# Kernel tuning notes

Hardware: AMD Instinct MI355X
Metric: run time of the kernel (lower is better)

Reference implementation:

```python
import jax, jax.numpy as jnp
import numpy as np

B, S, D, H = 8, 2048, 1024, 4
HD = D // H


def _layernorm(x, w, b, eps=1e-5):
    mu = jnp.mean(x, axis=-1, keepdims=True)
    var = jnp.mean((x - mu) ** 2, axis=-1, keepdims=True)
    return (x - mu) * jax.lax.rsqrt(var + eps) * w + b


def setup_inputs() -> dict:
    key = jax.random.key(0)
    ks = jax.random.split(key, 10)
    s = 1.0 / np.sqrt(D)
    return {
        "text_representation": jax.random.normal(ks[0], (B, S, D), jnp.float32),
        "image_representation": jax.random.normal(ks[1], (B, S, D), jnp.float32),
        "ln_t_w": jnp.ones((D,), jnp.float32),
        "ln_t_b": jnp.zeros((D,), jnp.float32),
        "ln_i_w": jnp.ones((D,), jnp.float32),
        "ln_i_b": jnp.zeros((D,), jnp.float32),
        "Wa": jax.random.uniform(ks[2], (H, HD, D), jnp.float32, -s, s),
        "Wa_b": jax.random.uniform(ks[3], (H, HD), jnp.float32, -s, s),
        "Wq": jax.random.uniform(ks[4], (H, HD, D), jnp.float32, -s, s),
        "Wq_b": jax.random.uniform(ks[5], (H, HD), jnp.float32, -s, s),
        "sim_w": jax.random.uniform(ks[6], (HD, 1), jnp.float32, -1.0, 1.0),
        "sim_b": jax.random.uniform(ks[7], (HD,), jnp.float32, -1.0, 1.0),
        "fc_w": jax.random.uniform(ks[8], (1, H * HD), jnp.float32, -s, s),
        "fc_b": jax.random.uniform(ks[9], (1,), jnp.float32, -s, s),
    }


def reference(text_representation, image_representation, ln_t_w, ln_t_b,
              ln_i_w, ln_i_b, Wa, Wa_b, Wq, Wq_b, sim_w, sim_b, fc_w, fc_b):
    eps_cos = 1e-6
    text_rep = _layernorm(text_representation, ln_t_w, ln_t_b)   # [B,S,D]
    image_rep = _layernorm(image_representation, ln_i_w, ln_i_b)  # [B,S,D]
    # cosine similarity along last dim (torch-style norm clamping)
    tn = jnp.maximum(jnp.linalg.norm(text_rep, axis=-1), eps_cos)
    im = jnp.maximum(jnp.linalg.norm(image_rep, axis=-1), eps_cos)
    per_pos_sim = jnp.sum(text_rep * image_rep, axis=-1) / (tn * im)  # [B,S]
    global_sim = jnp.mean(per_pos_sim, axis=1, keepdims=True)          # [B,1]
    text_global = jnp.mean(text_rep, axis=1)    # [B,D]
    image_global = jnp.mean(image_rep, axis=1)  # [B,D]
    gate_a = jnp.einsum('bd,hkd->bhk', text_global, Wa) + Wa_b    # [B,H,HD]
    gate_q = jnp.einsum('bd,hkd->bhk', image_global, Wq) + Wq_b   # [B,H,HD]
    sim_feat = global_sim * sim_w[:, 0] + sim_b                   # [B,HD]
    gates = jax.nn.relu(gate_a + gate_q + sim_feat[:, None, :])   # [B,H,HD]
    combined = gates.reshape(gates.shape[0], H * HD)              # [B,H*HD]
    final_gate = jax.nn.sigmoid(combined @ fc_w.T + fc_b)         # [B,1]
    g = final_gate[:, :, None]                                    # [B,1,1]
    return g * text_rep + (1.0 - g) * image_rep
```

## Files before the change

kernel.cpp:

```cpp
#include <hip/hip_runtime.h>
#include <math.h>

#define BB 8
#define SS 2048
#define DD 1024
#define HH 4
#define HDD 256
#define NROW (BB*SS)

#define GG 32
#define NBLK (NROW/GG)

#define OFF_TG    0
#define OFF_IG    (BB*DD)
#define OFF_SIM   (2*BB*DD)
#define OFF_LOGIT (OFF_SIM + BB)
#define OFF_CNT   (OFF_LOGIT + BB)
#define WS_CLEAR  (OFF_CNT + 2)

#define GF 8
#define NSLF (NROW/GF)
#define F_MU_T 0
#define F_RS_T NROW
#define F_MU_I (2*NROW)
#define F_RS_I (3*NROW)
#define F_PT   (4*NROW)
#define F_PI   (F_PT + NSLF*DD)
#define F_PS   (F_PI + NSLF*DD)
#define F_TG   (F_PS + NSLF)
#define F_IG   (F_TG + BB*DD)
#define F_SIM  (F_IG + BB*DD)
#define F_LOGIT (F_SIM + BB)

__device__ __forceinline__ float wred(float v) {
#pragma unroll
  for (int m = 32; m > 0; m >>= 1) v += __shfl_xor(v, m, 64);
  return v;
}
__device__ __forceinline__ float hsum(const float4 v) { return v.x+v.y+v.z+v.w; }
__device__ __forceinline__ float hsq(const float4 v)  { return v.x*v.x+v.y*v.y+v.z*v.z+v.w*v.w; }
__device__ __forceinline__ float hdot(const float4 a, const float4 b) {
  return a.x*b.x + a.y*b.y + a.z*b.z + a.w*b.w;
}

__global__ __launch_bounds__(256, 2) void fused(
    const float* __restrict__ text, const float* __restrict__ image,
    const float* __restrict__ wt, const float* __restrict__ bt,
    const float* __restrict__ wi, const float* __restrict__ bi,
    const float* __restrict__ Wa, const float* __restrict__ Wab,
    const float* __restrict__ Wq, const float* __restrict__ Wqb,
    const float* __restrict__ simw, const float* __restrict__ simb,
    const float* __restrict__ fcw, const float* __restrict__ fcb,
    float* __restrict__ ws, float* __restrict__ out)
{
  const int blk  = blockIdx.x;
  const int tid  = threadIdx.x;
  const int lane = tid & 63;
  const int wv   = tid >> 6;
  const int row0 = blk * GG;
  const int b    = blk >> 6;

  __shared__ float smu_t[GG], srs_t[GG], smu_i[GG], srs_i[GG];
  __shared__ float sAcc[2][4][DD];
  __shared__ float ssim[4];
  __shared__ float red3[4][4][BB];

  int* c1 = (int*)(ws + OFF_CNT);
  int* c2 = c1 + 1;

  {
    const int cb = lane << 2;
    float4 Wt[4], Bt[4], Wi4[4], Bi4[4];
#pragma unroll
    for (int j = 0; j < 4; ++j) {
      Wt[j]  = *(const float4*)(wt + j*256 + cb);
      Bt[j]  = *(const float4*)(bt + j*256 + cb);
      Wi4[j] = *(const float4*)(wi + j*256 + cb);
      Bi4[j] = *(const float4*)(bi + j*256 + cb);
    }
    float4 tga[4], iga[4];
#pragma unroll
    for (int j = 0; j < 4; ++j) {
      tga[j] = make_float4(0.f,0.f,0.f,0.f);
      iga[j] = make_float4(0.f,0.f,0.f,0.f);
    }
    float sim_loc = 0.f;
    const float invD = 1.f/DD;
    const int rbase = row0 + wv*8;

    float4 tb[2][4], ib[2][4];
    {
      const float* tr = text  + (size_t)rbase*DD + cb;
      const float* ir = image + (size_t)rbase*DD + cb;
#pragma unroll
      for (int j = 0; j < 4; ++j) {
        tb[0][j] = *(const float4*)(tr + j*256);
        ib[0][j] = *(const float4*)(ir + j*256);
      }
    }

#pragma unroll 2
    for (int r = 0; r < 8; ++r) {
      const int cur = r & 1, nxt = cur ^ 1;
      if (r < 7) {
        const float* tr = text  + (size_t)(rbase + r + 1)*DD + cb;
        const float* ir = image + (size_t)(rbase + r + 1)*DD + cb;
#pragma unroll
        for (int j = 0; j < 4; ++j) {
          tb[nxt][j] = *(const float4*)(tr + j*256);
          ib[nxt][j] = *(const float4*)(ir + j*256);
        }
      }

      float st=0.f, qt=0.f, si=0.f, qi=0.f;
#pragma unroll
      for (int j = 0; j < 4; ++j) {
        st += hsum(tb[cur][j]);  qt += hsq(tb[cur][j]);
        si += hsum(ib[cur][j]);  qi += hsq(ib[cur][j]);
      }
      st = wred(st); qt = wred(qt); si = wred(si); qi = wred(qi);
      const float mt = st*invD, rt = rsqrtf(qt*invD - mt*mt + 1e-5f);
      const float mi = si*invD, ri = rsqrtf(qi*invD - mi*mi + 1e-5f);
      if (lane == 0) {
        smu_t[wv*8+r]=mt; srs_t[wv*8+r]=rt;
        smu_i[wv*8+r]=mi; srs_i[wv*8+r]=ri;
      }

      float dot=0.f, nt=0.f, ni=0.f;
#pragma unroll
      for (int j = 0; j < 4; ++j) {
        float4 tn, iv;
        tn.x = (tb[cur][j].x-mt)*rt*Wt[j].x + Bt[j].x;
        tn.y = (tb[cur][j].y-mt)*rt*Wt[j].y + Bt[j].y;
        tn.z = (tb[cur][j].z-mt)*rt*Wt[j].z + Bt[j].z;
        tn.w = (tb[cur][j].w-mt)*rt*Wt[j].w + Bt[j].w;
        iv.x = (ib[cur][j].x-mi)*ri*Wi4[j].x + Bi4[j].x;
        iv.y = (ib[cur][j].y-mi)*ri*Wi4[j].y + Bi4[j].y;
        iv.z = (ib[cur][j].z-mi)*ri*Wi4[j].z + Bi4[j].z;
        iv.w = (ib[cur][j].w-mi)*ri*Wi4[j].w + Bi4[j].w;
        tga[j].x += tn.x; tga[j].y += tn.y; tga[j].z += tn.z; tga[j].w += tn.w;
        iga[j].x += iv.x; iga[j].y += iv.y; iga[j].z += iv.z; iga[j].w += iv.w;
        dot += hdot(tn, iv); nt += hsq(tn); ni += hsq(iv);
      }
      dot = wred(dot); nt = wred(nt); ni = wred(ni);
      sim_loc += dot / (fmaxf(sqrtf(nt),1e-6f) * fmaxf(sqrtf(ni),1e-6f));
    }

#pragma unroll
    for (int j = 0; j < 4; ++j) {
      *(float4*)&sAcc[0][wv][j*256 + cb] = tga[j];
      *(float4*)&sAcc[1][wv][j*256 + cb] = iga[j];
    }
    if (lane == 0) ssim[wv] = sim_loc;
    __syncthreads();

    const int c0 = tid << 2;
    float4 vt = make_float4(0.f,0.f,0.f,0.f);
    float4 vi = make_float4(0.f,0.f,0.f,0.f);
#pragma unroll
    for (int w = 0; w < 4; ++w) {
      const float4 a = *(const float4*)&sAcc[0][w][c0];
      vt.x += a.x; vt.y += a.y; vt.z += a.z; vt.w += a.w;
      const float4 e = *(const float4*)&sAcc[1][w][c0];
      vi.x += e.x; vi.y += e.y; vi.z += e.z; vi.w += e.w;
    }
    atomicAdd(&ws[OFF_TG + b*DD + c0 + 0], vt.x);
    atomicAdd(&ws[OFF_TG + b*DD + c0 + 1], vt.y);
    atomicAdd(&ws[OFF_TG + b*DD + c0 + 2], vt.z);
    atomicAdd(&ws[OFF_TG + b*DD + c0 + 3], vt.w);
    atomicAdd(&ws[OFF_IG + b*DD + c0 + 0], vi.x);
    atomicAdd(&ws[OFF_IG + b*DD + c0 + 1], vi.y);
    atomicAdd(&ws[OFF_IG + b*DD + c0 + 2], vi.z);
    atomicAdd(&ws[OFF_IG + b*DD + c0 + 3], vi.w);
    if (tid == 0) {
      atomicAdd(&ws[OFF_SIM + b], ssim[0]+ssim[1]+ssim[2]+ssim[3]);
    }
  }

  __syncthreads();
  if (tid == 0) {
    __hip_atomic_fetch_add(c1, 1, __ATOMIC_RELEASE, __HIP_MEMORY_SCOPE_AGENT);
  }

  if (blk < 256) {
    if (tid == 0) {
      while (__hip_atomic_load(c1, __ATOMIC_RELAXED, __HIP_MEMORY_SCOPE_AGENT) < NBLK)
        __builtin_amdgcn_s_sleep(8);
      __threadfence();
    }
    __syncthreads();

    const int d0 = tid << 2;
    const int r0 = blk * 4;
    for (int rr = 0; rr < 4; ++rr) {
      const int r = r0 + rr;
      const float4 a4 = *(const float4*)(Wa + (size_t)r*DD + d0);
      const float4 q4 = *(const float4*)(Wq + (size_t)r*DD + d0);
      float acc[BB];
#pragma unroll
      for (int bq = 0; bq < BB; ++bq) {
        const float4 t = *(const float4*)(ws + OFF_TG + bq*DD + d0);
        const float4 i = *(const float4*)(ws + OFF_IG + bq*DD + d0);
        acc[bq] = hdot(a4, t) + hdot(q4, i);
      }
#pragma unroll
      for (int bq = 0; bq < BB; ++bq) {
        acc[bq] = wred(acc[bq]);
        if (lane == 0) red3[rr][wv][bq] = acc[bq];
      }
    }
    __syncthreads();
    if (tid < BB) {
      const int bq = tid;
      const float inv = 1.f/SS;
      const float gs = ws[OFF_SIM + bq] * inv;
      float part = 0.f;
#pragma unroll
      for (int rr = 0; rr < 4; ++rr) {
        const int r = r0 + rr;
        const int k = r & 255;
        const float v = (red3[rr][0][bq] + red3[rr][1][bq] + red3[rr][2][bq] + red3[rr][3][bq]) * inv;
        float gate = v + Wab[r] + Wqb[r] + gs*simw[k] + simb[k];
        gate = fmaxf(gate, 0.f);
        part += gate * fcw[r];
      }
      atomicAdd(&ws[OFF_LOGIT + bq], part);
    }
    __syncthreads();
    if (tid == 0) {
      __hip_atomic_fetch_add(c2, 1, __ATOMIC_RELEASE, __HIP_MEMORY_SCOPE_AGENT);
    }
  }

  if (tid == 0) {
    while (__hip_atomic_load(c2, __ATOMIC_RELAXED, __HIP_MEMORY_SCOPE_AGENT) < 256)
      __builtin_amdgcn_s_sleep(8);
    __threadfence();
  }
  __syncthreads();

  {
    const int d0 = tid << 2;
    const float4 wt4 = *(const float4*)(wt + d0);
    const float4 bt4 = *(const float4*)(bt + d0);
    const float4 wi4 = *(const float4*)(wi + d0);
    const float4 bi4 = *(const float4*)(bi + d0);
    const float g  = 1.f / (1.f + expf(-(ws[OFF_LOGIT + b] + fcb[0])));
    const float gi = 1.f - g;

    float4 tg[2][4], ig[2][4];
#pragma unroll
    for (int r = 0; r < 4; ++r) {
      tg[0][r] = *(const float4*)(text  + (size_t)(row0+r)*DD + d0);
      ig[0][r] = *(const float4*)(image + (size_t)(row0+r)*DD + d0);
    }
#pragma unroll 2
    for (int gidx = 0; gidx < 8; ++gidx) {
      const int cur = gidx & 1, nxt = cur ^ 1;
      if (gidx < 7) {
        const int nr = row0 + (gidx+1)*4;
#pragma unroll
        for (int r = 0; r < 4; ++r) {
          tg[nxt][r] = *(const float4*)(text  + (size_t)(nr+r)*DD + d0);
          ig[nxt][r] = *(const float4*)(image + (size_t)(nr+r)*DD + d0);
        }
      }
      const int rr = gidx*4;
#pragma unroll
      for (int r = 0; r < 4; ++r) {
        const float mt = smu_t[rr+r], rt = srs_t[rr+r];
        const float mi = smu_i[rr+r], ri = srs_i[rr+r];
        const float gt = g*rt, gii = gi*ri;
        float4 o;
        o.x = gt*(tg[cur][r].x-mt)*wt4.x + g*bt4.x + gii*(ig[cur][r].x-mi)*wi4.x + gi*bi4.x;
        o.y = gt*(tg[cur][r].y-mt)*wt4.y + g*bt4.y + gii*(ig[cur][r].y-mi)*wi4.y + gi*bi4.y;
        o.z = gt*(tg[cur][r].z-mt)*wt4.z + g*bt4.z + gii*(ig[cur][r].z-mi)*wi4.z + gi*bi4.z;
        o.w = gt*(tg[cur][r].w-mt)*wt4.w + g*bt4.w + gii*(ig[cur][r].w-mi)*wi4.w + gi*bi4.w;
        *(float4*)(out + (size_t)(row0+rr+r)*DD + d0) = o;
      }
    }
  }
}

__global__ __launch_bounds__(256) void k1_stats(
    const float* __restrict__ text, const float* __restrict__ image,
    const float* __restrict__ wt, const float* __restrict__ bt,
    const float* __restrict__ wi, const float* __restrict__ bi,
    float* __restrict__ ws)
{
  const int g    = blockIdx.x;
  const int tid  = threadIdx.x;
  const int lane = tid & 63;
  const int wv   = tid >> 6;
  const int d0   = tid << 2;
  const int row0 = g * GF;

  __shared__ float red1[4][8];
  __shared__ float red2[4][6];

  const float4 wt4 = *(const float4*)(wt + d0);
  const float4 bt4 = *(const float4*)(bt + d0);
  const float4 wi4 = *(const float4*)(wi + d0);
  const float4 bi4 = *(const float4*)(bi + d0);

  float4 tga = make_float4(0.f,0.f,0.f,0.f);
  float4 iga = make_float4(0.f,0.f,0.f,0.f);
  float sim_loc = 0.f;

  for (int r = 0; r < GF; r += 2) {
    const size_t base0 = (size_t)(row0 + r) * DD + d0;
    const size_t base1 = base0 + DD;
    const float4 t0 = *(const float4*)(text  + base0);
    const float4 i0 = *(const float4*)(image + base0);
    const float4 t1 = *(const float4*)(text  + base1);
    const float4 i1 = *(const float4*)(image + base1);

    float a0 = hsum(t0), a1 = hsq(t0), a2 = hsum(i0), a3 = hsq(i0);
    float a4 = hsum(t1), a5 = hsq(t1), a6 = hsum(i1), a7 = hsq(i1);
    a0 = wred(a0); a1 = wred(a1); a2 = wred(a2); a3 = wred(a3);
    a4 = wred(a4); a5 = wred(a5); a6 = wred(a6); a7 = wred(a7);
    if (lane == 0) {
      red1[wv][0]=a0; red1[wv][1]=a1; red1[wv][2]=a2; red1[wv][3]=a3;
      red1[wv][4]=a4; red1[wv][5]=a5; red1[wv][6]=a6; red1[wv][7]=a7;
    }
    __syncthreads();
    float s[8];
#pragma unroll
    for (int q = 0; q < 8; ++q) s[q] = red1[0][q]+red1[1][q]+red1[2][q]+red1[3][q];
    const float invD = 1.f/DD;
    const float mt0 = s[0]*invD, rt0 = rsqrtf(s[1]*invD - mt0*mt0 + 1e-5f);
    const float mi0 = s[2]*invD, ri0 = rsqrtf(s[3]*invD - mi0*mi0 + 1e-5f);
    const float mt1 = s[4]*invD, rt1 = rsqrtf(s[5]*invD - mt1*mt1 + 1e-5f);
    const float mi1 = s[6]*invD, ri1 = rsqrtf(s[7]*invD - mi1*mi1 + 1e-5f);
    if (tid == 0) {
      const int row = row0 + r;
      ws[F_MU_T+row]=mt0;   ws[F_RS_T+row]=rt0;
      ws[F_MU_I+row]=mi0;   ws[F_RS_I+row]=ri0;
      ws[F_MU_T+row+1]=mt1; ws[F_RS_T+row+1]=rt1;
      ws[F_MU_I+row+1]=mi1; ws[F_RS_I+row+1]=ri1;
    }
    float4 tn0, in0, tn1, in1;
    tn0.x = (t0.x-mt0)*rt0*wt4.x + bt4.x;  tn0.y = (t0.y-mt0)*rt0*wt4.y + bt4.y;
    tn0.z = (t0.z-mt0)*rt0*wt4.z + bt4.z;  tn0.w = (t0.w-mt0)*rt0*wt4.w + bt4.w;
    in0.x = (i0.x-mi0)*ri0*wi4.x + bi4.x;  in0.y = (i0.y-mi0)*ri0*wi4.y + bi4.y;
    in0.z = (i0.z-mi0)*ri0*wi4.z + bi4.z;  in0.w = (i0.w-mi0)*ri0*wi4.w + bi4.w;
    tn1.x = (t1.x-mt1)*rt1*wt4.x + bt4.x;  tn1.y = (t1.y-mt1)*rt1*wt4.y + bt4.y;
    tn1.z = (t1.z-mt1)*rt1*wt4.z + bt4.z;  tn1.w = (t1.w-mt1)*rt1*wt4.w + bt4.w;
    in1.x = (i1.x-mi1)*ri1*wi4.x + bi4.x;  in1.y = (i1.y-mi1)*ri1*wi4.y + bi4.y;
    in1.z = (i1.z-mi1)*ri1*wi4.z + bi4.z;  in1.w = (i1.w-mi1)*ri1*wi4.w + bi4.w;

    tga.x += tn0.x + tn1.x; tga.y += tn0.y + tn1.y;
    tga.z += tn0.z + tn1.z; tga.w += tn0.w + tn1.w;
    iga.x += in0.x + in1.x; iga.y += in0.y + in1.y;
    iga.z += in0.z + in1.z; iga.w += in0.w + in1.w;

    float b0 = hdot(tn0,in0), b1 = hsq(tn0), b2 = hsq(in0);
    float b3 = hdot(tn1,in1), b4 = hsq(tn1), b5 = hsq(in1);
    b0 = wred(b0); b1 = wred(b1); b2 = wred(b2);
    b3 = wred(b3); b4 = wred(b4); b5 = wred(b5);
    if (lane == 0) {
      red2[wv][0]=b0; red2[wv][1]=b1; red2[wv][2]=b2;
      red2[wv][3]=b3; red2[wv][4]=b4; red2[wv][5]=b5;
    }
    __syncthreads();
    if (tid == 0) {
      float u[6];
#pragma unroll
      for (int q = 0; q < 6; ++q) u[q] = red2[0][q]+red2[1][q]+red2[2][q]+red2[3][q];
      sim_loc += u[0] / (fmaxf(sqrtf(u[1]),1e-6f) * fmaxf(sqrtf(u[2]),1e-6f));
      sim_loc += u[3] / (fmaxf(sqrtf(u[4]),1e-6f) * fmaxf(sqrtf(u[5]),1e-6f));
    }
  }
  *(float4*)(ws + F_PT + (size_t)g*DD + d0) = tga;
  *(float4*)(ws + F_PI + (size_t)g*DD + d0) = iga;
  if (tid == 0) ws[F_PS + g] = sim_loc;
}

__global__ __launch_bounds__(256) void kR_reduce(float* __restrict__ ws)
{
  const int tid = threadIdx.x;
  if (blockIdx.x < 256) {
    const int b   = blockIdx.x >> 5;
    const int ch  = blockIdx.x & 31;
    const int cl  = tid & 31;
    const int sg  = tid >> 5;
    const int col = ch*32 + cl;
    const float* pt = ws + F_PT + (size_t)(b*256 + sg*32)*DD + col;
    const float* pi = ws + F_PI + (size_t)(b*256 + sg*32)*DD + col;
    float at = 0.f, ai = 0.f;
#pragma unroll 4
    for (int k = 0; k < 32; ++k) {
      at += pt[(size_t)k*DD];
      ai += pi[(size_t)k*DD];
    }
    __shared__ float sred[2][8][32];
    sred[0][sg][cl] = at;
    sred[1][sg][cl] = ai;
    __syncthreads();
    if (tid < 32) {
      float v = 0.f;
#pragma unroll
      for (int q = 0; q < 8; ++q) v += sred[0][q][tid];
      ws[F_TG + b*DD + ch*32 + tid] = v;
    } else if (tid < 64) {
      const int c = tid - 32;
      float v = 0.f;
#pragma unroll
      for (int q = 0; q < 8; ++q) v += sred[1][q][c];
      ws[F_IG + b*DD + ch*32 + c] = v;
    }
  } else {
    __shared__ float sred[256];
    const int b = tid >> 5, j = tid & 31;
    float a = 0.f;
#pragma unroll
    for (int k = 0; k < 8; ++k) a += ws[F_PS + b*256 + j*8 + k];
    sred[tid] = a;
    __syncthreads();
    if (j == 0) {
      float s = 0.f;
#pragma unroll
      for (int m = 0; m < 32; ++m) s += sred[b*32 + m];
      ws[F_SIM + b] = s;
    }
    if (tid < BB) ws[F_LOGIT + tid] = 0.f;
  }
}

__global__ __launch_bounds__(256) void k2_gates(
    const float* __restrict__ Wa, const float* __restrict__ Wab,
    const float* __restrict__ Wq, const float* __restrict__ Wqb,
    const float* __restrict__ simw, const float* __restrict__ simb,
    const float* __restrict__ fcw, float* __restrict__ ws)
{
  const int tid  = threadIdx.x;
  const int lane = tid & 63;
  const int wv   = tid >> 6;
  const int r0   = blockIdx.x * 4;
  const int d0   = tid << 2;

  __shared__ float red[4][4][BB];

  for (int rr = 0; rr < 4; ++rr) {
    const int r = r0 + rr;
    const float4 a4 = *(const float4*)(Wa + (size_t)r*DD + d0);
    const float4 q4 = *(const float4*)(Wq + (size_t)r*DD + d0);
    float acc[BB];
#pragma unroll
    for (int b = 0; b < BB; ++b) {
      const float4 t = *(const float4*)(ws + F_TG + b*DD + d0);
      const float4 i = *(const float4*)(ws + F_IG + b*DD + d0);
      acc[b] = hdot(a4, t) + hdot(q4, i);
    }
#pragma unroll
    for (int b = 0; b < BB; ++b) {
      acc[b] = wred(acc[b]);
      if (lane == 0) red[rr][wv][b] = acc[b];
    }
  }
  __syncthreads();
  if (tid < BB) {
    const int b = tid;
    const float inv = 1.f/SS;
    const float gs = ws[F_SIM + b] * inv;
    float part = 0.f;
#pragma unroll
    for (int rr = 0; rr < 4; ++rr) {
      const int r = r0 + rr;
      const int k = r & 255;
      const float v = (red[rr][0][b] + red[rr][1][b] + red[rr][2][b] + red[rr][3][b]) * inv;
      float gate = v + Wab[r] + Wqb[r] + gs*simw[k] + simb[k];
      gate = fmaxf(gate, 0.f);
      part += gate * fcw[r];
    }
    atomicAdd(&ws[F_LOGIT + b], part);
  }
}

__global__ __launch_bounds__(256) void k3_blend(
    const float* __restrict__ text, const float* __restrict__ image,
    const float* __restrict__ wt, const float* __restrict__ bt,
    const float* __restrict__ wi, const float* __restrict__ bi,
    const float* __restrict__ fcb,
    const float* __restrict__ ws, float* __restrict__ out)
{
  const int r0 = blockIdx.x * 4;
  const int b  = r0 >> 11;
  const int d0 = threadIdx.x << 2;

  float4 t[4], im[4];
#pragma unroll
  for (int r = 0; r < 4; ++r) {
    t[r]  = *(const float4*)(text  + (size_t)(r0+r)*DD + d0);
    im[r] = *(const float4*)(image + (size_t)(r0+r)*DD + d0);
  }
  const float4 wt4 = *(const float4*)(wt + d0);
  const float4 bt4 = *(const float4*)(bt + d0);
  const float4 wi4 = *(const float4*)(wi + d0);
  const float4 bi4 = *(const float4*)(bi + d0);

  const float g  = 1.f / (1.f + expf(-(ws[F_LOGIT+b] + fcb[0])));
  const float gi = 1.f - g;

#pragma unroll
  for (int r = 0; r < 4; ++r) {
    const float mt = ws[F_MU_T+r0+r], rt = ws[F_RS_T+r0+r];
    const float mi = ws[F_MU_I+r0+r], ri = ws[F_RS_I+r0+r];
    const float gt = g*rt, gii = gi*ri;
    float4 o;
    o.x = gt*(t[r].x-mt)*wt4.x + g*bt4.x + gii*(im[r].x-mi)*wi4.x + gi*bi4.x;
    o.y = gt*(t[r].y-mt)*wt4.y + g*bt4.y + gii*(im[r].y-mi)*wi4.y + gi*bi4.y;
    o.z = gt*(t[r].z-mt)*wt4.z + g*bt4.z + gii*(im[r].z-mi)*wi4.z + gi*bi4.z;
    o.w = gt*(t[r].w-mt)*wt4.w + g*bt4.w + gii*(im[r].w-mi)*wi4.w + gi*bi4.w;
    *(float4*)(out + (size_t)(r0+r)*DD + d0) = o;
  }
}

extern "C" void kernel_launch(void* const* d_in, const int* in_sizes, int n_in,
                              void* d_out, int out_size, void* d_ws, size_t ws_size,
                              hipStream_t stream)
{
  const float* text   = (const float*)d_in[0];
  const float* image  = (const float*)d_in[1];
  const float* ln_t_w = (const float*)d_in[2];
  const float* ln_t_b = (const float*)d_in[3];
  const float* ln_i_w = (const float*)d_in[4];
  const float* ln_i_b = (const float*)d_in[5];
  const float* Wa     = (const float*)d_in[6];
  const float* Wab    = (const float*)d_in[7];
  const float* Wq     = (const float*)d_in[8];
  const float* Wqb    = (const float*)d_in[9];
  const float* simw   = (const float*)d_in[10];
  const float* simb   = (const float*)d_in[11];
  const float* fcw    = (const float*)d_in[12];
  const float* fcb    = (const float*)d_in[13];
  float* ws  = (float*)d_ws;
  float* out = (float*)d_out;

  hipMemsetAsync(ws, 0, WS_CLEAR * sizeof(float), stream);

  static int use_coop = -1;
  if (use_coop != 0) {
    void* args[16] = {
      (void*)&text, (void*)&image, (void*)&ln_t_w, (void*)&ln_t_b,
      (void*)&ln_i_w, (void*)&ln_i_b, (void*)&Wa, (void*)&Wab,
      (void*)&Wq, (void*)&Wqb, (void*)&simw, (void*)&simb,
      (void*)&fcw, (void*)&fcb, (void*)&ws, (void*)&out
    };
    hipError_t e = hipLaunchCooperativeKernel((void*)fused, dim3(NBLK), dim3(256),
                                              args, 0, stream);
    if (e == hipSuccess) { use_coop = 1; return; }
    use_coop = 0;
  }

  k1_stats<<<NSLF, 256, 0, stream>>>(text, image, ln_t_w, ln_t_b, ln_i_w, ln_i_b, ws);
  kR_reduce<<<257, 256, 0, stream>>>(ws);
  k2_gates<<<HH*HDD/4, 256, 0, stream>>>(Wa, Wab, Wq, Wqb, simw, simb, fcw, ws);
  k3_blend<<<NROW/4, 256, 0, stream>>>(text, image, ln_t_w, ln_t_b, ln_i_w, ln_i_b, fcb, ws, out);
}
```

Measured before the change: 248.4 us.

## Replace global atomic accumulation with per-block partials and a parallel grid reduction phase

Each block now writes its column sums and similarity partial to its own slot with plain relaxed stores instead of atomically adding into shared per-batch accumulators, which removes heavy atomic contention (512 blocks × 2048 atomics). A new phase has 256 blocks reduce the partials per batch and column chunk, while one extra block reduces the similarity partials. This adds a third grid-wide barrier. The first text/image loads of the final pass are now issued before waiting on the logit barrier, so they overlap the gate computation. The memset now clears only a small header.

```diff
diff --git a/kernel.cpp b/kernel.cpp
--- a/kernel.cpp
+++ b/kernel.cpp
@@ -11,12 +11,15 @@
 #define GG 32
 #define NBLK (NROW/GG)
 
-#define OFF_TG    0
-#define OFF_IG    (BB*DD)
-#define OFF_SIM   (2*BB*DD)
-#define OFF_LOGIT (OFF_SIM + BB)
-#define OFF_CNT   (OFF_LOGIT + BB)
-#define WS_CLEAR  (OFF_CNT + 2)
+#define OFF_LOGIT 0
+#define OFF_CNT   8
+#define HDRCLR    16
+#define OFF_TG    16
+#define OFF_IG    (OFF_TG + BB*DD)
+#define OFF_SIM   (OFF_IG + BB*DD)
+#define OFF_PT    32768
+#define OFF_PI    (OFF_PT + NBLK*DD)
+#define OFF_PS    (OFF_PI + NBLK*DD)
 
 #define GF 8
 #define NSLF (NROW/GF)
@@ -41,6 +44,9 @@
 __device__ __forceinline__ float hsq(const float4 v)  { return v.x*v.x+v.y*v.y+v.z*v.z+v.w*v.w; }
 __device__ __forceinline__ float hdot(const float4 a, const float4 b) {
   return a.x*b.x + a.y*b.y + a.z*b.z + a.w*b.w;
+}
+__device__ __forceinline__ void ast(float* p, float v) {
+  __hip_atomic_store(p, v, __ATOMIC_RELAXED, __HIP_MEMORY_SCOPE_AGENT);
 }
 
 __global__ __launch_bounds__(256, 2) void fused(
@@ -64,9 +70,11 @@
   __shared__ float sAcc[2][4][DD];
   __shared__ float ssim[4];
   __shared__ float red3[4][4][BB];
+  __shared__ float sred[2][8][32];
 
   int* c1 = (int*)(ws + OFF_CNT);
   int* c2 = c1 + 1;
+  int* c3 = c1 + 2;
 
   {
     const int cb = lane << 2;
@@ -164,17 +172,11 @@
       const float4 e = *(const float4*)&sAcc[1][w][c0];
       vi.x += e.x; vi.y += e.y; vi.z += e.z; vi.w += e.w;
     }
-    atomicAdd(&ws[OFF_TG + b*DD + c0 + 0], vt.x);
-    atomicAdd(&ws[OFF_TG + b*DD + c0 + 1], vt.y);
-    atomicAdd(&ws[OFF_TG + b*DD + c0 + 2], vt.z);
-    atomicAdd(&ws[OFF_TG + b*DD + c0 + 3], vt.w);
-    atomicAdd(&ws[OFF_IG + b*DD + c0 + 0], vi.x);
-    atomicAdd(&ws[OFF_IG + b*DD + c0 + 1], vi.y);
-    atomicAdd(&ws[OFF_IG + b*DD + c0 + 2], vi.z);
-    atomicAdd(&ws[OFF_IG + b*DD + c0 + 3], vi.w);
-    if (tid == 0) {
-      atomicAdd(&ws[OFF_SIM + b], ssim[0]+ssim[1]+ssim[2]+ssim[3]);
-    }
+    float* pt = ws + OFF_PT + (size_t)blk*DD + c0;
+    float* pi = ws + OFF_PI + (size_t)blk*DD + c0;
+    ast(pt+0, vt.x); ast(pt+1, vt.y); ast(pt+2, vt.z); ast(pt+3, vt.w);
+    ast(pi+0, vi.x); ast(pi+1, vi.y); ast(pi+2, vi.z); ast(pi+3, vi.w);
+    if (tid == 0) ast(ws + OFF_PS + blk, ssim[0]+ssim[1]+ssim[2]+ssim[3]);
   }
 
   __syncthreads();
@@ -185,6 +187,70 @@
   if (blk < 256) {
     if (tid == 0) {
       while (__hip_atomic_load(c1, __ATOMIC_RELAXED, __HIP_MEMORY_SCOPE_AGENT) < NBLK)
+        __builtin_amdgcn_s_sleep(8);
+      __threadfence();
+    }
+    __syncthreads();
+
+    const int b2  = blk >> 5;
+    const int ch  = blk & 31;
+    const int cl  = tid & 31;
+    const int sg  = tid >> 5;
+    const int col = ch*32 + cl;
+    const float* pt = ws + OFF_PT + (size_t)(b2*64 + sg*8)*DD + col;
+    const float* pi = ws + OFF_PI + (size_t)(b2*64 + sg*8)*DD + col;
+    float at = 0.f, ai = 0.f;
+#pragma unroll
+    for (int k = 0; k < 8; ++k) {
+      at += pt[(size_t)k*DD];
+      ai += pi[(size_t)k*DD];
+    }
+    sred[0][sg][cl] = at;
+    sred[1][sg][cl] = ai;
+    __syncthreads();
+    if (tid < 32) {
+      float v = 0.f;
+#pragma unroll
+      for (int q = 0; q < 8; ++q) v += sred[0][q][tid];
+      ast(&ws[OFF_TG + b2*DD + ch*32 + tid], v);
+    } else if (tid < 64) {
+      const int c = tid - 32;
+      float v = 0.f;
+#pragma unroll
+      for (int q = 0; q < 8; ++q) v += sred[1][q][c];
+      ast(&ws[OFF_IG + b2*DD + ch*32 + c], v);
+    }
+    __syncthreads();
+    if (tid == 0) {
+      __hip_atomic_fetch_add(c2, 1, __ATOMIC_RELEASE, __HIP_MEMORY_SCOPE_AGENT);
+    }
+  } else if (blk == 256) {
+    if (tid == 0) {
+      while (__hip_atomic_load(c1, __ATOMIC_RELAXED, __HIP_MEMORY_SCOPE_AGENT) < NBLK)
+        __builtin_amdgcn_s_sleep(8);
+      __threadfence();
+    }
+    __syncthreads();
+    float* sflat = (float*)sred;
+    const int b3 = tid >> 5, j = tid & 31;
+    const float a = ws[OFF_PS + b3*64 + j*2] + ws[OFF_PS + b3*64 + j*2 + 1];
+    sflat[tid] = a;
+    __syncthreads();
+    if (j == 0) {
+      float s = 0.f;
+#pragma unroll
+      for (int m = 0; m < 32; ++m) s += sflat[b3*32 + m];
+      ast(&ws[OFF_SIM + b3], s);
+    }
+    __syncthreads();
+    if (tid == 0) {
+      __hip_atomic_fetch_add(c2, 1, __ATOMIC_RELEASE, __HIP_MEMORY_SCOPE_AGENT);
+    }
+  }
+
+  if (blk < 256) {
+    if (tid == 0) {
+      while (__hip_atomic_load(c2, __ATOMIC_RELAXED, __HIP_MEMORY_SCOPE_AGENT) < 257)
         __builtin_amdgcn_s_sleep(8);
       __threadfence();
     }
@@ -228,16 +294,9 @@
     }
     __syncthreads();
     if (tid == 0) {
-      __hip_atomic_fetch_add(c2, 1, __ATOMIC_RELEASE, __HIP_MEMORY_SCOPE_AGENT);
-    }
-  }
-
-  if (tid == 0) {
-    while (__hip_atomic_load(c2, __ATOMIC_RELAXED, __HIP_MEMORY_SCOPE_AGENT) < 256)
-      __builtin_amdgcn_s_sleep(8);
-    __threadfence();
-  }
-  __syncthreads();
+      __hip_atomic_fetch_add(c3, 1, __ATOMIC_RELEASE, __HIP_MEMORY_SCOPE_AGENT);
+    }
+  }
 
   {
     const int d0 = tid << 2;
@@ -245,15 +304,23 @@
     const float4 bt4 = *(const float4*)(bt + d0);
     const float4 wi4 = *(const float4*)(wi + d0);
     const float4 bi4 = *(const float4*)(bi + d0);
-    const float g  = 1.f / (1.f + expf(-(ws[OFF_LOGIT + b] + fcb[0])));
-    const float gi = 1.f - g;
-
     float4 tg[2][4], ig[2][4];
 #pragma unroll
     for (int r = 0; r < 4; ++r) {
       tg[0][r] = *(const float4*)(text  + (size_t)(row0+r)*DD + d0);
       ig[0][r] = *(const float4*)(image + (size_t)(row0+r)*DD + d0);
     }
+
+    if (tid == 0) {
+      while (__hip_atomic_load(c3, __ATOMIC_RELAXED, __HIP_MEMORY_SCOPE_AGENT) < 256)
+        __builtin_amdgcn_s_sleep(8);
+      __threadfence();
+    }
+    __syncthreads();
+
+    const float g  = 1.f / (1.f + expf(-(ws[OFF_LOGIT + b] + fcb[0])));
+    const float gi = 1.f - g;
+
 #pragma unroll 2
     for (int gidx = 0; gidx < 8; ++gidx) {
       const int cur = gidx & 1, nxt = cur ^ 1;
@@ -537,7 +604,7 @@
   float* ws  = (float*)d_ws;
   float* out = (float*)d_out;
 
-  hipMemsetAsync(ws, 0, WS_CLEAR * sizeof(float), stream);
+  hipMemsetAsync(ws, 0, HDRCLR * sizeof(float), stream);
 
   static int use_coop = -1;
   if (use_coop != 0) {
```

Measured after the change: 244.0 us. Within noise of the previous version (-1.7%).

## Replace global atomics and grid barriers with per-batch partials and counters

Applied to the files above, without the earlier changes.

Each block now writes its per-column text/image sums and similarity partials to its own workspace slot with plain stores, replacing the contended float atomicAdds. The grid-wide barriers become per-batch counters. 32 blocks (4 per batch) each reduce their batch's 64 partials and compute a quarter of the gate logits. The apply phase waits only for its own batch's gate, and the first row loads are issued before that wait. This removes global atomic contention and the full-grid synchronisation. In exchange it adds a larger workspace footprint and concentrates the gate GEMV on 32 blocks, each reading 256 weight rows serially.

```diff
diff --git a/kernel.cpp b/kernel.cpp
--- a/kernel.cpp
+++ b/kernel.cpp
@@ -11,12 +11,12 @@
 #define GG 32
 #define NBLK (NROW/GG)
 
-#define OFF_TG    0
-#define OFF_IG    (BB*DD)
-#define OFF_SIM   (2*BB*DD)
-#define OFF_LOGIT (OFF_SIM + BB)
-#define OFF_CNT   (OFF_LOGIT + BB)
-#define WS_CLEAR  (OFF_CNT + 2)
+#define OFF_LOGIT 0
+#define OFF_CNT   8
+#define HDRCLR    24
+#define OFF_PS    32
+#define OFF_PT    1024
+#define OFF_PI    (OFF_PT + NBLK*DD)
 
 #define GF 8
 #define NSLF (NROW/GF)
@@ -41,6 +41,9 @@
 __device__ __forceinline__ float hsq(const float4 v)  { return v.x*v.x+v.y*v.y+v.z*v.z+v.w*v.w; }
 __device__ __forceinline__ float hdot(const float4 a, const float4 b) {
   return a.x*b.x + a.y*b.y + a.z*b.z + a.w*b.w;
+}
+__device__ __forceinline__ void ast(float* p, float v) {
+  __hip_atomic_store(p, v, __ATOMIC_RELAXED, __HIP_MEMORY_SCOPE_AGENT);
 }
 
 __global__ __launch_bounds__(256, 2) void fused(
@@ -63,20 +66,21 @@
   __shared__ float smu_t[GG], srs_t[GG], smu_i[GG], srs_i[GG];
   __shared__ float sAcc[2][4][DD];
   __shared__ float ssim[4];
-  __shared__ float red3[4][4][BB];
-
-  int* c1 = (int*)(ws + OFF_CNT);
-  int* c2 = c1 + 1;
+  __shared__ float sgp[4];
+  __shared__ float sGS;
+
+  int* cb = (int*)(ws + OFF_CNT);
+  int* gd = cb + 8;
 
   {
-    const int cb = lane << 2;
+    const int cb4 = lane << 2;
     float4 Wt[4], Bt[4], Wi4[4], Bi4[4];
 #pragma unroll
     for (int j = 0; j < 4; ++j) {
-      Wt[j]  = *(const float4*)(wt + j*256 + cb);
-      Bt[j]  = *(const float4*)(bt + j*256 + cb);
-      Wi4[j] = *(const float4*)(wi + j*256 + cb);
-      Bi4[j] = *(const float4*)(bi + j*256 + cb);
+      Wt[j]  = *(const float4*)(wt + j*256 + cb4);
+      Bt[j]  = *(const float4*)(bt + j*256 + cb4);
+      Wi4[j] = *(const float4*)(wi + j*256 + cb4);
+      Bi4[j] = *(const float4*)(bi + j*256 + cb4);
     }
     float4 tga[4], iga[4];
 #pragma unroll
@@ -90,8 +94,8 @@
 
     float4 tb[2][4], ib[2][4];
     {
-      const float* tr = text  + (size_t)rbase*DD + cb;
-      const float* ir = image + (size_t)rbase*DD + cb;
+      const float* tr = text  + (size_t)rbase*DD + cb4;
+      const float* ir = image + (size_t)rbase*DD + cb4;
 #pragma unroll
       for (int j = 0; j < 4; ++j) {
         tb[0][j] = *(const float4*)(tr + j*256);
@@ -103,8 +107,8 @@
     for (int r = 0; r < 8; ++r) {
       const int cur = r & 1, nxt = cur ^ 1;
       if (r < 7) {
-        const float* tr = text  + (size_t)(rbase + r + 1)*DD + cb;
-        const float* ir = image + (size_t)(rbase + r + 1)*DD + cb;
+        const float* tr = text  + (size_t)(rbase + r + 1)*DD + cb4;
+        const float* ir = image + (size_t)(rbase + r + 1)*DD + cb4;
 #pragma unroll
         for (int j = 0; j < 4; ++j) {
           tb[nxt][j] = *(const float4*)(tr + j*256);
@@ -148,8 +152,8 @@
 
 #pragma unroll
     for (int j = 0; j < 4; ++j) {
-      *(float4*)&sAcc[0][wv][j*256 + cb] = tga[j];
-      *(float4*)&sAcc[1][wv][j*256 + cb] = iga[j];
+      *(float4*)&sAcc[0][wv][j*256 + cb4] = tga[j];
+      *(float4*)&sAcc[1][wv][j*256 + cb4] = iga[j];
     }
     if (lane == 0) ssim[wv] = sim_loc;
     __syncthreads();
@@ -164,80 +168,84 @@
       const float4 e = *(const float4*)&sAcc[1][w][c0];
       vi.x += e.x; vi.y += e.y; vi.z += e.z; vi.w += e.w;
     }
-    atomicAdd(&ws[OFF_TG + b*DD + c0 + 0], vt.x);
-    atomicAdd(&ws[OFF_TG + b*DD + c0 + 1], vt.y);
-    atomicAdd(&ws[OFF_TG + b*DD + c0 + 2], vt.z);
-    atomicAdd(&ws[OFF_TG + b*DD + c0 + 3], vt.w);
-    atomicAdd(&ws[OFF_IG + b*DD + c0 + 0], vi.x);
-    atomicAdd(&ws[OFF_IG + b*DD + c0 + 1], vi.y);
-    atomicAdd(&ws[OFF_IG + b*DD + c0 + 2], vi.z);
-    atomicAdd(&ws[OFF_IG + b*DD + c0 + 3], vi.w);
-    if (tid == 0) {
-      atomicAdd(&ws[OFF_SIM + b], ssim[0]+ssim[1]+ssim[2]+ssim[3]);
-    }
+    float* pt = ws + OFF_PT + (size_t)blk*DD + c0;
+    float* pi = ws + OFF_PI + (size_t)blk*DD + c0;
+    ast(pt+0, vt.x); ast(pt+1, vt.y); ast(pt+2, vt.z); ast(pt+3, vt.w);
+    ast(pi+0, vi.x); ast(pi+1, vi.y); ast(pi+2, vi.z); ast(pi+3, vi.w);
+    if (tid == 0) ast(ws + OFF_PS + blk, ssim[0]+ssim[1]+ssim[2]+ssim[3]);
   }
 
   __syncthreads();
   if (tid == 0) {
-    __hip_atomic_fetch_add(c1, 1, __ATOMIC_RELEASE, __HIP_MEMORY_SCOPE_AGENT);
-  }
-
-  if (blk < 256) {
+    __hip_atomic_fetch_add(&cb[b], 1, __ATOMIC_RELEASE, __HIP_MEMORY_SCOPE_AGENT);
+  }
+
+  if (blk < 32) {
+    const int gb = blk >> 2;
+    const int q  = blk & 3;
     if (tid == 0) {
-      while (__hip_atomic_load(c1, __ATOMIC_RELAXED, __HIP_MEMORY_SCOPE_AGENT) < NBLK)
+      while (__hip_atomic_load(&cb[gb], __ATOMIC_RELAXED, __HIP_MEMORY_SCOPE_AGENT) < 64)
         __builtin_amdgcn_s_sleep(8);
       __threadfence();
     }
     __syncthreads();
 
-    const int d0 = tid << 2;
-    const int r0 = blk * 4;
-    for (int rr = 0; rr < 4; ++rr) {
-      const int r = r0 + rr;
-      const float4 a4 = *(const float4*)(Wa + (size_t)r*DD + d0);
-      const float4 q4 = *(const float4*)(Wq + (size_t)r*DD + d0);
-      float acc[BB];
-#pragma unroll
-      for (int bq = 0; bq < BB; ++bq) {
-        const float4 t = *(const float4*)(ws + OFF_TG + bq*DD + d0);
-        const float4 i = *(const float4*)(ws + OFF_IG + bq*DD + d0);
-        acc[bq] = hdot(a4, t) + hdot(q4, i);
-      }
-#pragma unroll
-      for (int bq = 0; bq < BB; ++bq) {
-        acc[bq] = wred(acc[bq]);
-        if (lane == 0) red3[rr][wv][bq] = acc[bq];
-      }
-    }
-    __syncthreads();
-    if (tid < BB) {
-      const int bq = tid;
+    float* sTG = &sAcc[0][0][0];
+    float* sIG = &sAcc[0][1][0];
+    {
+      const int c0 = tid << 2;
+      const float* pt = ws + OFF_PT + (size_t)(gb*64)*DD + c0;
+      const float* pi = ws + OFF_PI + (size_t)(gb*64)*DD + c0;
+      float4 vt = make_float4(0.f,0.f,0.f,0.f);
+      float4 vi = make_float4(0.f,0.f,0.f,0.f);
+#pragma unroll 8
+      for (int s = 0; s < 64; ++s) {
+        const float4 a = *(const float4*)(pt + (size_t)s*DD);
+        vt.x += a.x; vt.y += a.y; vt.z += a.z; vt.w += a.w;
+        const float4 e = *(const float4*)(pi + (size_t)s*DD);
+        vi.x += e.x; vi.y += e.y; vi.z += e.z; vi.w += e.w;
+      }
+      *(float4*)&sTG[c0] = vt;
+      *(float4*)&sIG[c0] = vi;
+      if (wv == 0) {
+        float s = ws[OFF_PS + gb*64 + lane];
+        s = wred(s);
+        if (lane == 0) sGS = s * (1.f/SS);
+      }
+    }
+    __syncthreads();
+
+    {
+      const int cb4 = lane << 2;
       const float inv = 1.f/SS;
-      const float gs = ws[OFF_SIM + bq] * inv;
+      const float gs = sGS;
       float part = 0.f;
-#pragma unroll
-      for (int rr = 0; rr < 4; ++rr) {
-        const int r = r0 + rr;
-        const int k = r & 255;
-        const float v = (red3[rr][0][bq] + red3[rr][1][bq] + red3[rr][2][bq] + red3[rr][3][bq]) * inv;
-        float gate = v + Wab[r] + Wqb[r] + gs*simw[k] + simb[k];
-        gate = fmaxf(gate, 0.f);
-        part += gate * fcw[r];
-      }
-      atomicAdd(&ws[OFF_LOGIT + bq], part);
+      for (int i = 0; i < 64; ++i) {
+        const int r = q*256 + wv*64 + i;
+        float acc = 0.f;
+#pragma unroll
+        for (int j = 0; j < 4; ++j) {
+          const float4 a4 = *(const float4*)(Wa + (size_t)r*DD + j*256 + cb4);
+          const float4 q4 = *(const float4*)(Wq + (size_t)r*DD + j*256 + cb4);
+          const float4 t4 = *(const float4*)&sTG[j*256 + cb4];
+          const float4 i4 = *(const float4*)&sIG[j*256 + cb4];
+          acc += hdot(a4, t4) + hdot(q4, i4);
+        }
+        acc = wred(acc);
+        if (lane == 0) {
+          const int k = r & 255;
+          float gate = acc*inv + Wab[r] + Wqb[r] + gs*simw[k] + simb[k];
+          part += fmaxf(gate, 0.f) * fcw[r];
+        }
+      }
+      if (lane == 0) sgp[wv] = part;
     }
     __syncthreads();
     if (tid == 0) {
-      __hip_atomic_fetch_add(c2, 1, __ATOMIC_RELEASE, __HIP_MEMORY_SCOPE_AGENT);
-    }
-  }
-
-  if (tid == 0) {
-    while (__hip_atomic_load(c2, __ATOMIC_RELAXED, __HIP_MEMORY_SCOPE_AGENT) < 256)
-      __builtin_amdgcn_s_sleep(8);
-    __threadfence();
-  }
-  __syncthreads();
+      atomicAdd(&ws[OFF_LOGIT + gb], sgp[0]+sgp[1]+sgp[2]+sgp[3]);
+      __hip_atomic_fetch_add(&gd[gb], 1, __ATOMIC_RELEASE, __HIP_MEMORY_SCOPE_AGENT);
+    }
+  }
 
   {
     const int d0 = tid << 2;
@@ -245,15 +253,23 @@
     const float4 bt4 = *(const float4*)(bt + d0);
     const float4 wi4 = *(const float4*)(wi + d0);
     const float4 bi4 = *(const float4*)(bi + d0);
-    const float g  = 1.f / (1.f + expf(-(ws[OFF_LOGIT + b] + fcb[0])));
-    const float gi = 1.f - g;
-
     float4 tg[2][4], ig[2][4];
 #pragma unroll
     for (int r = 0; r < 4; ++r) {
       tg[0][r] = *(const float4*)(text  + (size_t)(row0+r)*DD + d0);
       ig[0][r] = *(const float4*)(image + (size_t)(row0+r)*DD + d0);
     }
+
+    if (tid == 0) {
+      while (__hip_atomic_load(&gd[b], __ATOMIC_RELAXED, __HIP_MEMORY_SCOPE_AGENT) < 4)
+        __builtin_amdgcn_s_sleep(8);
+      __threadfence();
+    }
+    __syncthreads();
+
+    const float g  = 1.f / (1.f + expf(-(ws[OFF_LOGIT + b] + fcb[0])));
+    const float gi = 1.f - g;
+
 #pragma unroll 2
     for (int gidx = 0; gidx < 8; ++gidx) {
       const int cur = gidx & 1, nxt = cur ^ 1;
@@ -537,7 +553,7 @@
   float* ws  = (float*)d_ws;
   float* out = (float*)d_out;
 
-  hipMemsetAsync(ws, 0, WS_CLEAR * sizeof(float), stream);
+  hipMemsetAsync(ws, 0, HDRCLR * sizeof(float), stream);
 
   static int use_coop = -1;
   if (use_coop != 0) {
```

Measured after the change: 246.4 us. No clear change (-0.8%).
